# Optimization experiments

Measured on AMD Instinct MI355X. Metric: run time of the kernel, lower is better.

Reference implementation:

```python
import jax, jax.numpy as jnp
import numpy as np

HIDDEN = 4096
N_HEADS = 32
N_KV_HEADS = 8
HEAD_DIM = HIDDEN // N_HEADS  # 128
ROPE_THETA = 10000.0
B, S = 2, 2048


def apply_rope_neox(x, positions, theta=ROPE_THETA):
    # x: [B, S, H, D], positions: [S]
    d = x.shape[-1]
    inv_freq = 1.0 / (theta ** (jnp.arange(0, d, 2, dtype=jnp.float32) / d))  # [D/2]
    freqs = positions.astype(jnp.float32)[:, None] * inv_freq                # [S, D/2]
    cos = jnp.cos(freqs)[None, :, None, :]                                   # [1,S,1,D/2]
    sin = jnp.sin(freqs)[None, :, None, :]
    x1, x2 = x[..., : d // 2], x[..., d // 2 :]
    return jnp.concatenate([x1 * cos - x2 * sin, x2 * cos + x1 * sin], axis=-1).astype(x.dtype)


def setup_inputs() -> dict:
    key = jax.random.key(0)
    k1, k2, k3 = jax.random.split(key, 3)
    positions = jnp.arange(S, dtype=jnp.int64) if jax.config.jax_enable_x64 else jnp.arange(S, dtype=jnp.int32)
    hidden_states = jax.random.normal(k1, (B, S, HIDDEN), dtype=jnp.float32)
    q_size = N_HEADS * HEAD_DIM
    kv_size = N_KV_HEADS * HEAD_DIM
    w_qkv = jax.random.normal(k2, (HIDDEN, q_size + 2 * kv_size), dtype=jnp.float32) * (HIDDEN ** -0.5)
    w_o = jax.random.normal(k3, (q_size, HIDDEN), dtype=jnp.float32) * (q_size ** -0.5)
    return {"positions": positions, "hidden_states": hidden_states, "w_qkv": w_qkv, "w_o": w_o}


def reference(positions, hidden_states, w_qkv, w_o):
    q_size = N_HEADS * HEAD_DIM
    kv_size = N_KV_HEADS * HEAD_DIM
    scaling = HEAD_DIM ** -0.5

    # Fused QKV projection
    qkv = jnp.einsum('bsh,hm->bsm', hidden_states, w_qkv)
    q = qkv[..., :q_size].reshape(B, S, N_HEADS, HEAD_DIM)
    k = qkv[..., q_size : q_size + kv_size].reshape(B, S, N_KV_HEADS, HEAD_DIM)
    v = qkv[..., q_size + kv_size :].reshape(B, S, N_KV_HEADS, HEAD_DIM)

    # Neox-style RoPE on q, k
    q = apply_rope_neox(q, positions)
    k = apply_rope_neox(k, positions)

    # GQA: repeat kv heads to match query heads
    rep = N_HEADS // N_KV_HEADS
    k = jnp.repeat(k, rep, axis=2)  # [B,S,Hq,D]
    v = jnp.repeat(v, rep, axis=2)

    # Causal attention (prefill path of PagedAttention)
    scores = jnp.einsum('bqhd,bkhd->bhqk', q, k) * scaling  # [B,H,S,S]
    causal = jnp.tril(jnp.ones((S, S), dtype=bool))
    scores = jnp.where(causal[None, None], scores, jnp.finfo(scores.dtype).min)
    probs = jax.nn.softmax(scores, axis=-1)
    attn = jnp.einsum('bhqk,bkhd->bqhd', probs, v).reshape(B, S, q_size)

    # Output projection
    out = jnp.einsum('bsm,mh->bsh', attn, w_o)
    return out
```

## Files before the change

kernel.cpp:

```cpp
#include <hip/hip_runtime.h>

#define S_LEN 2048
#define NB 2
#define NH 32
#define NKV 8
#define HD 128
#define HID 4096
#define NQKV 6144

using bf16x8 = __attribute__((ext_vector_type(8))) __bf16;
using f32x4  = __attribute__((ext_vector_type(4))) float;

__device__ __forceinline__ ushort f2b(float f) {
  uint u = __builtin_bit_cast(uint, f);
  u += 0x7fffu + ((u >> 16) & 1u);
  return (ushort)(u >> 16);
}
__device__ __forceinline__ float b2f(ushort h) {
  uint u = ((uint)h) << 16;
  return __builtin_bit_cast(float, u);
}

__device__ __forceinline__ uint cvt_pk_bf16(float lo, float hi) {
  uint r;
  asm("v_cvt_pk_bf16_f32 %0, %1, %2" : "=v"(r) : "v"(lo), "v"(hi));
  return r;
}

__device__ __forceinline__ void gld16(const void* g, void* l) {
  __builtin_amdgcn_global_load_lds((const __attribute__((address_space(1))) void*)g,
                                   (__attribute__((address_space(3))) void*)l, 16, 0, 0);
}

__device__ __forceinline__ void stc(float* C, size_t i, float v)  { C[i] = v; }
__device__ __forceinline__ void stc(ushort* C, size_t i, float v) { C[i] = f2b(v); }

__global__ void cvt_bf16(const float* __restrict__ src, ushort* __restrict__ dst, int n) {
  int i = (blockIdx.x * 256 + threadIdx.x) * 4;
  if (i < n) {
    float4 v = *(const float4*)(src + i);
    *(ushort4*)(dst + i) = make_ushort4(f2b(v.x), f2b(v.y), f2b(v.z), f2b(v.w));
  }
}

__global__ void trans_f32_bf16(const float* __restrict__ src, ushort* __restrict__ dst,
                               int R, int C) {
  __shared__ float tile[32][33];
  const int c0 = blockIdx.x * 32, r0 = blockIdx.y * 32;
  const int x = threadIdx.x, y = threadIdx.y;
#pragma unroll
  for (int i = 0; i < 32; i += 8)
    tile[y + i][x] = src[(size_t)(r0 + y + i) * C + (c0 + x)];
  __syncthreads();
#pragma unroll
  for (int i = 0; i < 32; i += 8)
    dst[(size_t)(c0 + y + i) * R + (r0 + x)] = f2b(tile[x][y + i]);
}

template <typename OutT>
__global__ __launch_bounds__(256) void gemm_nt(const ushort* __restrict__ A,
                                               const ushort* __restrict__ Bt,
                                               OutT* __restrict__ C,
                                               int M, int N, int K, int lda, int ldb) {
  __shared__ ushort As[128 * 32];
  __shared__ ushort Bs[128 * 32];
  const int tid  = threadIdx.x;
  const int wave = tid >> 6;
  const int lane = tid & 63;
  const int lr = lane & 15, lg = lane >> 4;
  const int m0 = blockIdx.y * 128, n0 = blockIdx.x * 128;
  const int wm = (wave >> 1) * 64, wn = (wave & 1) * 64;

  f32x4 acc[4][4];
#pragma unroll
  for (int i = 0; i < 4; ++i)
#pragma unroll
    for (int j = 0; j < 4; ++j) acc[i][j] = (f32x4){0.f, 0.f, 0.f, 0.f};

  for (int kt = 0; kt < K; kt += 32) {
    __syncthreads();
#pragma unroll
    for (int it = 0; it < 2; ++it) {
      const int cbase = it * 256 + wave * 64;
      const int c = cbase + lane;
      const int row = c >> 2, kc = c & 3;
      gld16(A  + (size_t)(m0 + row) * lda + kt + kc * 8, As + cbase * 8);
      gld16(Bt + (size_t)(n0 + row) * ldb + kt + kc * 8, Bs + cbase * 8);
    }
    __syncthreads();
    bf16x8 af[4], bfg[4];
#pragma unroll
    for (int i = 0; i < 4; ++i) {
      af[i]  = *(const bf16x8*)(As + (wm + i * 16 + lr) * 32 + lg * 8);
      bfg[i] = *(const bf16x8*)(Bs + (wn + i * 16 + lr) * 32 + lg * 8);
    }
#pragma unroll
    for (int i = 0; i < 4; ++i)
#pragma unroll
      for (int j = 0; j < 4; ++j)
        acc[i][j] = __builtin_amdgcn_mfma_f32_16x16x32_bf16(af[i], bfg[j], acc[i][j], 0, 0, 0);
  }

#pragma unroll
  for (int i = 0; i < 4; ++i)
#pragma unroll
    for (int j = 0; j < 4; ++j)
#pragma unroll
      for (int r = 0; r < 4; ++r) {
        const int row = m0 + wm + i * 16 + lg * 4 + r;
        const int col = n0 + wn + j * 16 + lr;
        stc(C, (size_t)row * N + col, acc[i][j][r]);
      }
}

__global__ __launch_bounds__(256) void rope_qk(ushort* __restrict__ qkv) {
  int t = blockIdx.x * 256 + threadIdx.x;
  const int i = t & 63;
  t >>= 6;
  const int head  = t % (NH + NKV);
  const int token = t / (NH + NKV);
  const int s = token & (S_LEN - 1);
  const size_t base = (size_t)token * NQKV + (head < NH ? head * HD : HID + (head - NH) * HD);
  const float x1 = b2f(qkv[base + i]);
  const float x2 = b2f(qkv[base + 64 + i]);
  const float invf = exp2f(-(float)i * 0.2076205059304602f);
  const float fr = (float)s * invf;
  float cs, sn;
  sincosf(fr, &sn, &cs);
  float o1 = x1 * cs - x2 * sn;
  float o2 = x2 * cs + x1 * sn;
  if (head < NH) {
    o1 *= 0.08838834764831845f;
    o2 *= 0.08838834764831845f;
  }
  qkv[base + i]      = f2b(o1);
  qkv[base + 64 + i] = f2b(o2);
}

__global__ void vtrans(const ushort* __restrict__ qkv, ushort* __restrict__ Vt) {
  __shared__ ushort tile[32][33];
  const int dt = blockIdx.x * 32, st = blockIdx.y * 32, bk = blockIdx.z;
  const int b = bk >> 3, kv = bk & 7;
  const int x = threadIdx.x, y = threadIdx.y;
#pragma unroll
  for (int i = 0; i < 32; i += 8)
    tile[y + i][x] =
        qkv[(size_t)(b * S_LEN + st + y + i) * NQKV + 5120 + kv * HD + dt + x];
  __syncthreads();
#pragma unroll
  for (int i = 0; i < 32; i += 8)
    Vt[((size_t)bk * HD + dt + y + i) * S_LEN + st + x] = tile[x][y + i];
}

__global__ __launch_bounds__(256) void attn_fa(ushort* __restrict__ qkv,
                                               const ushort* __restrict__ Vt) {
  const int lin = blockIdx.x + 32 * blockIdx.y + 256 * blockIdx.z;
  const int swz = (lin & 7) * 64 + (lin >> 3);
  const int qp = swz & 31;
  const int g  = swz >> 5;
  const int kvh = g & 7;
  const int b   = g >> 3;

  const int wid  = threadIdx.x >> 6;
  const int lane = threadIdx.x & 63;
  const int lr = lane & 15, lg = lane >> 4;
  const int h  = kvh * 4 + wid;

  const ushort* K = qkv + (size_t)(b * S_LEN) * NQKV + HID + kvh * HD;
  const ushort* V = Vt + (size_t)(b * NKV + kvh) * (HD * S_LEN);

  __shared__ ushort P[4][2][16 * 40];

  for (int seg = 0; seg < 2; ++seg) {
    const int qt = seg ? (63 - qp) : qp;
    const int q0 = qt * 32;
    const ushort* Q = qkv + (size_t)(b * S_LEN + q0) * NQKV + h * HD;

    bf16x8 qf[2][4];
#pragma unroll
    for (int t = 0; t < 2; ++t)
#pragma unroll
      for (int kb = 0; kb < 4; ++kb)
        qf[t][kb] = *(const bf16x8*)(Q + (size_t)(t * 16 + lr) * NQKV + kb * 32 + lg * 8);

    f32x4 o[2][8];
#pragma unroll
    for (int t = 0; t < 2; ++t)
#pragma unroll
      for (int c = 0; c < 8; ++c) o[t][c] = (f32x4){0.f, 0.f, 0.f, 0.f};
    float mi[2]  = {-1e30f, -1e30f};
    float lip[2] = {0.f, 0.f};

    for (int k0 = 0; k0 <= q0; k0 += 32) {
      bf16x8 kf[2][4];
#pragma unroll
      for (int kb = 0; kb < 4; ++kb) {
        kf[0][kb] = *(const bf16x8*)(K + (size_t)(k0 + lr) * NQKV + kb * 32 + lg * 8);
        kf[1][kb] = *(const bf16x8*)(K + (size_t)(k0 + 16 + lr) * NQKV + kb * 32 + lg * 8);
      }
      bf16x8 vf[8];
#pragma unroll
      for (int c = 0; c < 8; ++c)
        vf[c] = *(const bf16x8*)(V + (size_t)(c * 16 + lr) * S_LEN + k0 + lg * 8);

      f32x4 s[2][2];
#pragma unroll
      for (int t = 0; t < 2; ++t)
#pragma unroll
        for (int u = 0; u < 2; ++u) s[t][u] = (f32x4){0.f, 0.f, 0.f, 0.f};

      __builtin_amdgcn_s_setprio(1);
#pragma unroll
      for (int kb = 0; kb < 4; ++kb) {
        s[0][0] = __builtin_amdgcn_mfma_f32_16x16x32_bf16(kf[0][kb], qf[0][kb], s[0][0], 0, 0, 0);
        s[1][0] = __builtin_amdgcn_mfma_f32_16x16x32_bf16(kf[0][kb], qf[1][kb], s[1][0], 0, 0, 0);
        s[0][1] = __builtin_amdgcn_mfma_f32_16x16x32_bf16(kf[1][kb], qf[0][kb], s[0][1], 0, 0, 0);
        s[1][1] = __builtin_amdgcn_mfma_f32_16x16x32_bf16(kf[1][kb], qf[1][kb], s[1][1], 0, 0, 0);
      }
      __builtin_amdgcn_s_setprio(0);

      if (k0 == q0) {
#pragma unroll
        for (int t = 0; t < 2; ++t)
#pragma unroll
          for (int u = 0; u < 2; ++u)
#pragma unroll
            for (int r = 0; r < 4; ++r)
              if (u * 16 + lg * 4 + r > t * 16 + lr) s[t][u][r] = -1e30f;
      }

      float pm[2];
#pragma unroll
      for (int t = 0; t < 2; ++t) {
        float a = fmaxf(fmaxf(s[t][0][0], s[t][0][1]), fmaxf(s[t][0][2], s[t][0][3]));
        float c = fmaxf(fmaxf(s[t][1][0], s[t][1][1]), fmaxf(s[t][1][2], s[t][1][3]));
        pm[t] = fmaxf(a, c);
      }

      if (__any((pm[0] > mi[0] + 8.f) || (pm[1] > mi[1] + 8.f))) {
#pragma unroll
        for (int t = 0; t < 2; ++t) {
          float m = pm[t];
          m = fmaxf(m, __shfl_xor(m, 16));
          m = fmaxf(m, __shfl_xor(m, 32));
          const float mn = fmaxf(mi[t], m);
          const float al = __expf(mi[t] - mn);
          mi[t] = mn;
          lip[t] *= al;
#pragma unroll
          for (int r = 0; r < 4; ++r) {
            const float ar = __shfl(al, lg * 4 + r);
#pragma unroll
            for (int c = 0; c < 8; ++c) o[t][c][r] *= ar;
          }
        }
      }

#pragma unroll
      for (int t = 0; t < 2; ++t) {
        float p[2][4];
#pragma unroll
        for (int u = 0; u < 2; ++u)
#pragma unroll
          for (int r = 0; r < 4; ++r) p[u][r] = __expf(s[t][u][r] - mi[t]);
        lip[t] += ((p[0][0] + p[0][1]) + (p[0][2] + p[0][3])) +
                  ((p[1][0] + p[1][1]) + (p[1][2] + p[1][3]));
        ushort* Pw = &P[wid][t][0];
#pragma unroll
        for (int u = 0; u < 2; ++u) {
          const uint w0 = cvt_pk_bf16(p[u][0], p[u][1]);
          const uint w1 = cvt_pk_bf16(p[u][2], p[u][3]);
          *(uint2*)(Pw + lr * 40 + u * 16 + lg * 4) = make_uint2(w0, w1);
        }
      }
      const bf16x8 pa0 = *(const bf16x8*)(&P[wid][0][0] + lr * 40 + lg * 8);
      const bf16x8 pa1 = *(const bf16x8*)(&P[wid][1][0] + lr * 40 + lg * 8);

      __builtin_amdgcn_s_setprio(1);
#pragma unroll
      for (int c = 0; c < 8; ++c) {
        o[0][c] = __builtin_amdgcn_mfma_f32_16x16x32_bf16(pa0, vf[c], o[0][c], 0, 0, 0);
        o[1][c] = __builtin_amdgcn_mfma_f32_16x16x32_bf16(pa1, vf[c], o[1][c], 0, 0, 0);
      }
      __builtin_amdgcn_s_setprio(0);
    }

    float linv[2];
#pragma unroll
    for (int t = 0; t < 2; ++t) {
      float rt = lip[t];
      rt += __shfl_xor(rt, 16);
      rt += __shfl_xor(rt, 32);
      linv[t] = 1.f / rt;
    }
#pragma unroll
    for (int t = 0; t < 2; ++t) {
#pragma unroll
      for (int r = 0; r < 4; ++r) {
        const float ir = __shfl(linv[t], lg * 4 + r);
        const size_t row = (size_t)(b * S_LEN + q0 + t * 16 + lg * 4 + r) * NQKV + h * HD;
#pragma unroll
        for (int c = 0; c < 8; ++c) qkv[row + c * 16 + lr] = f2b(o[t][c][r] * ir);
      }
    }
  }
}

extern "C" void kernel_launch(void* const* d_in, const int* in_sizes, int n_in,
                              void* d_out, int out_size, void* d_ws, size_t ws_size,
                              hipStream_t stream) {
  const float* hidden = (const float*)d_in[1];
  const float* w_qkv  = (const float*)d_in[2];
  const float* w_o    = (const float*)d_in[3];
  float* out = (float*)d_out;
  char* ws = (char*)d_ws;

  ushort* wqkvT = (ushort*)(ws);
  ushort* Vt    = (ushort*)(ws);
  ushort* hb    = (ushort*)(ws + (48u << 20));
  ushort* woT   = (ushort*)(ws + (48u << 20));
  ushort* qkvb  = (ushort*)(ws + (80u << 20));

  trans_f32_bf16<<<dim3(192, 128), dim3(32, 8), 0, stream>>>(w_qkv, wqkvT, HID, NQKV);
  cvt_bf16<<<16384, 256, 0, stream>>>(hidden, hb, NB * S_LEN * HID);
  gemm_nt<ushort><<<dim3(48, 32), 256, 0, stream>>>(
      hb, wqkvT, qkvb, NB * S_LEN, NQKV, HID, HID, HID);
  rope_qk<<<40960, 256, 0, stream>>>(qkvb);
  vtrans<<<dim3(4, 64, 16), dim3(32, 8), 0, stream>>>(qkvb, Vt);
  trans_f32_bf16<<<dim3(128, 128), dim3(32, 8), 0, stream>>>(w_o, woT, HID, HID);
  attn_fa<<<dim3(32, 8, 2), 256, 0, stream>>>(qkvb, Vt);
  gemm_nt<float><<<dim3(32, 32), 256, 0, stream>>>(
      qkvb, woT, out, NB * S_LEN, HID, HID, NQKV, HID);
}
```

Before: 953.3 us.

## Rewrite GEMM with double-buffered LDS, 128x256 tiles, swizzle, and XCD remap

Replaces the single-buffered 128x128 GEMM with a 512-thread 128x256-tile kernel. It double-buffers the LDS panels so the next K slice loads while MFMAs run, XOR-swizzles the LDS chunk layout to cut bank conflicts, and remaps workgroup IDs so neighbouring tiles land on the same XCD for L2 reuse. It also raises wave priority around the MFMA bursts. The costs are more LDS per block and a possibly lower tile count, fewer CUs busy, on the smaller output projection.

New measurement: 959.5 us. About the same (+0.6%).

```diff
diff --git a/kernel.cpp b/kernel.cpp
--- a/kernel.cpp
+++ b/kernel.cpp
@@ -57,19 +57,35 @@
     dst[(size_t)(c0 + y + i) * R + (r0 + x)] = f2b(tile[x][y + i]);
 }
 
+__device__ __forceinline__ void stage_panel(const ushort* __restrict__ src, int ld,
+                                            int row0, int kt, ushort* dst,
+                                            int nchunks, int wave, int lane) {
+  for (int cb = wave * 64; cb < nchunks; cb += 512) {
+    const int c = cb + lane;
+    const int row = c >> 2;
+    const int cg = (c & 3) ^ (row & 3);
+    gld16(src + (size_t)(row0 + row) * ld + kt + cg * 8, dst + cb * 8);
+  }
+}
+
 template <typename OutT>
-__global__ __launch_bounds__(256) void gemm_nt(const ushort* __restrict__ A,
-                                               const ushort* __restrict__ Bt,
-                                               OutT* __restrict__ C,
-                                               int M, int N, int K, int lda, int ldb) {
-  __shared__ ushort As[128 * 32];
-  __shared__ ushort Bs[128 * 32];
-  const int tid  = threadIdx.x;
-  const int wave = tid >> 6;
-  const int lane = tid & 63;
+__global__ __launch_bounds__(512, 4) void gemm_np(const ushort* __restrict__ A,
+                                                  const ushort* __restrict__ Bt,
+                                                  OutT* __restrict__ C,
+                                                  int M, int Ncol, int K,
+                                                  int lda, int ldb) {
+  __shared__ ushort As[2][128 * 32];
+  __shared__ ushort Bs[2][256 * 32];
+  const int tid = threadIdx.x, wave = tid >> 6, lane = tid & 63;
   const int lr = lane & 15, lg = lane >> 4;
-  const int m0 = blockIdx.y * 128, n0 = blockIdx.x * 128;
-  const int wm = (wave >> 1) * 64, wn = (wave & 1) * 64;
+  const int wm = wave >> 2, wn = wave & 3;
+
+  const int gx = gridDim.x;
+  const int nwg = gx * gridDim.y;
+  const int orig = blockIdx.y * gx + blockIdx.x;
+  const int q8 = nwg >> 3, r8 = nwg & 7, xcd = orig & 7, loc = orig >> 3;
+  const int wg = (xcd < r8 ? xcd * (q8 + 1) : r8 * (q8 + 1) + (xcd - r8) * q8) + loc;
+  const int n0 = (wg % gx) * 256, m0 = (wg / gx) * 128;
 
   f32x4 acc[4][4];
 #pragma unroll
@@ -77,28 +93,46 @@
 #pragma unroll
     for (int j = 0; j < 4; ++j) acc[i][j] = (f32x4){0.f, 0.f, 0.f, 0.f};
 
-  for (int kt = 0; kt < K; kt += 32) {
-    __syncthreads();
-#pragma unroll
-    for (int it = 0; it < 2; ++it) {
-      const int cbase = it * 256 + wave * 64;
-      const int c = cbase + lane;
-      const int row = c >> 2, kc = c & 3;
-      gld16(A  + (size_t)(m0 + row) * lda + kt + kc * 8, As + cbase * 8);
-      gld16(Bt + (size_t)(n0 + row) * ldb + kt + kc * 8, Bs + cbase * 8);
-    }
-    __syncthreads();
-    bf16x8 af[4], bfg[4];
-#pragma unroll
-    for (int i = 0; i < 4; ++i) {
-      af[i]  = *(const bf16x8*)(As + (wm + i * 16 + lr) * 32 + lg * 8);
-      bfg[i] = *(const bf16x8*)(Bs + (wn + i * 16 + lr) * 32 + lg * 8);
-    }
-#pragma unroll
-    for (int i = 0; i < 4; ++i)
-#pragma unroll
-      for (int j = 0; j < 4; ++j)
-        acc[i][j] = __builtin_amdgcn_mfma_f32_16x16x32_bf16(af[i], bfg[j], acc[i][j], 0, 0, 0);
+  const int foff = lr * 32 + ((lg ^ (lr & 3)) << 3);
+  const int NT = K >> 5;
+
+  stage_panel(A,  lda, m0, 0, As[0], 512, wave, lane);
+  stage_panel(Bt, ldb, n0, 0, Bs[0], 1024, wave, lane);
+  asm volatile("s_waitcnt vmcnt(0)" ::: "memory");
+  __builtin_amdgcn_s_barrier();
+
+  for (int it = 0; it < NT; ++it) {
+    const int buf = it & 1;
+    const bool more = (it + 1 < NT);
+    if (more) {
+      stage_panel(A,  lda, m0, (it + 1) << 5, As[buf ^ 1], 512, wave, lane);
+      stage_panel(Bt, ldb, n0, (it + 1) << 5, Bs[buf ^ 1], 1024, wave, lane);
+    }
+    const ushort* Ap = As[buf] + wm * (64 * 32);
+    const ushort* Bp = Bs[buf] + wn * (64 * 32);
+#pragma unroll
+    for (int q = 0; q < 4; ++q) {
+      const int qm = q & 1, qn = q >> 1;
+      bf16x8 af[2], bfr[2];
+#pragma unroll
+      for (int f = 0; f < 2; ++f)
+        af[f] = *(const bf16x8*)(Ap + (qm * 2 + f) * (16 * 32) + foff);
+#pragma unroll
+      for (int g = 0; g < 2; ++g)
+        bfr[g] = *(const bf16x8*)(Bp + (qn * 2 + g) * (16 * 32) + foff);
+      __builtin_amdgcn_s_setprio(1);
+#pragma unroll
+      for (int f = 0; f < 2; ++f)
+#pragma unroll
+        for (int g = 0; g < 2; ++g)
+          acc[qm * 2 + f][qn * 2 + g] = __builtin_amdgcn_mfma_f32_16x16x32_bf16(
+              af[f], bfr[g], acc[qm * 2 + f][qn * 2 + g], 0, 0, 0);
+      __builtin_amdgcn_s_setprio(0);
+    }
+    if (more) {
+      asm volatile("s_waitcnt vmcnt(0)" ::: "memory");
+      __builtin_amdgcn_s_barrier();
+    }
   }
 
 #pragma unroll
@@ -107,9 +141,9 @@
     for (int j = 0; j < 4; ++j)
 #pragma unroll
       for (int r = 0; r < 4; ++r) {
-        const int row = m0 + wm + i * 16 + lg * 4 + r;
-        const int col = n0 + wn + j * 16 + lr;
-        stc(C, (size_t)row * N + col, acc[i][j][r]);
+        const int row = m0 + wm * 64 + i * 16 + lg * 4 + r;
+        const int col = n0 + wn * 64 + j * 16 + lr;
+        stc(C, (size_t)row * Ncol + col, acc[i][j][r]);
       }
 }
 
@@ -323,12 +357,12 @@
 
   trans_f32_bf16<<<dim3(192, 128), dim3(32, 8), 0, stream>>>(w_qkv, wqkvT, HID, NQKV);
   cvt_bf16<<<16384, 256, 0, stream>>>(hidden, hb, NB * S_LEN * HID);
-  gemm_nt<ushort><<<dim3(48, 32), 256, 0, stream>>>(
+  gemm_np<ushort><<<dim3(24, 32), 512, 0, stream>>>(
       hb, wqkvT, qkvb, NB * S_LEN, NQKV, HID, HID, HID);
   rope_qk<<<40960, 256, 0, stream>>>(qkvb);
   vtrans<<<dim3(4, 64, 16), dim3(32, 8), 0, stream>>>(qkvb, Vt);
   trans_f32_bf16<<<dim3(128, 128), dim3(32, 8), 0, stream>>>(w_o, woT, HID, HID);
   attn_fa<<<dim3(32, 8, 2), 256, 0, stream>>>(qkvb, Vt);
-  gemm_nt<float><<<dim3(32, 32), 256, 0, stream>>>(
+  gemm_np<float><<<dim3(16, 32), 512, 0, stream>>>(
       qkvb, woT, out, NB * S_LEN, HID, HID, NQKV, HID);
 }
```

## Double-buffer GEMM LDS tiles with K=64 stages and XOR-swizzled layout

Applied to the files above, without the earlier changes.

Replaces the single-buffered K=32 GEMM with a double-buffered K=64 version. Global-to-LDS loads for the next tile are issued before compute on the current one, with a partial vmcnt wait and raw barriers in place of two __syncthreads per step. The LDS layout is XOR-swizzled to avoid bank conflicts, and MFMA issue gets a raised wave priority. LDS use grows to 64KB per block, which may limit occupancy, and the hand-placed waitcnt is fragile.

Result: faster. 855.4 us (-10.3%).

```diff
diff --git a/kernel.cpp b/kernel.cpp
--- a/kernel.cpp
+++ b/kernel.cpp
@@ -57,19 +57,33 @@
     dst[(size_t)(c0 + y + i) * R + (r0 + x)] = f2b(tile[x][y + i]);
 }
 
+__device__ __forceinline__ void stage_tile(const ushort* __restrict__ A,
+                                           const ushort* __restrict__ Bt,
+                                           int lda, int ldb, int m0, int n0, int kt,
+                                           ushort* dA, ushort* dB, int wave, int lane) {
+#pragma unroll
+  for (int h = 0; h < 4; ++h) {
+    const int cb = h * 256 + wave * 64;
+    const int c = cb + lane;
+    const int row = c >> 3;
+    const int kc = (c & 7) ^ (row & 7);
+    gld16(A  + (size_t)(m0 + row) * lda + kt + kc * 8, dA + cb * 8);
+    gld16(Bt + (size_t)(n0 + row) * ldb + kt + kc * 8, dB + cb * 8);
+  }
+}
+
 template <typename OutT>
-__global__ __launch_bounds__(256) void gemm_nt(const ushort* __restrict__ A,
-                                               const ushort* __restrict__ Bt,
-                                               OutT* __restrict__ C,
-                                               int M, int N, int K, int lda, int ldb) {
-  __shared__ ushort As[128 * 32];
-  __shared__ ushort Bs[128 * 32];
-  const int tid  = threadIdx.x;
-  const int wave = tid >> 6;
-  const int lane = tid & 63;
+__global__ __launch_bounds__(256, 2) void gemm_p2(const ushort* __restrict__ A,
+                                                  const ushort* __restrict__ Bt,
+                                                  OutT* __restrict__ C,
+                                                  int M, int Ncol, int K,
+                                                  int lda, int ldb) {
+  __shared__ ushort As[2][128 * 64];
+  __shared__ ushort Bs[2][128 * 64];
+  const int tid = threadIdx.x, wave = tid >> 6, lane = tid & 63;
   const int lr = lane & 15, lg = lane >> 4;
+  const int wm = wave >> 1, wn = wave & 1;
   const int m0 = blockIdx.y * 128, n0 = blockIdx.x * 128;
-  const int wm = (wave >> 1) * 64, wn = (wave & 1) * 64;
 
   f32x4 acc[4][4];
 #pragma unroll
@@ -77,39 +91,54 @@
 #pragma unroll
     for (int j = 0; j < 4; ++j) acc[i][j] = (f32x4){0.f, 0.f, 0.f, 0.f};
 
-  for (int kt = 0; kt < K; kt += 32) {
-    __syncthreads();
-#pragma unroll
-    for (int it = 0; it < 2; ++it) {
-      const int cbase = it * 256 + wave * 64;
-      const int c = cbase + lane;
-      const int row = c >> 2, kc = c & 3;
-      gld16(A  + (size_t)(m0 + row) * lda + kt + kc * 8, As + cbase * 8);
-      gld16(Bt + (size_t)(n0 + row) * ldb + kt + kc * 8, Bs + cbase * 8);
-    }
-    __syncthreads();
-    bf16x8 af[4], bfg[4];
-#pragma unroll
-    for (int i = 0; i < 4; ++i) {
-      af[i]  = *(const bf16x8*)(As + (wm + i * 16 + lr) * 32 + lg * 8);
-      bfg[i] = *(const bf16x8*)(Bs + (wn + i * 16 + lr) * 32 + lg * 8);
-    }
-#pragma unroll
-    for (int i = 0; i < 4; ++i)
-#pragma unroll
-      for (int j = 0; j < 4; ++j)
-        acc[i][j] = __builtin_amdgcn_mfma_f32_16x16x32_bf16(af[i], bfg[j], acc[i][j], 0, 0, 0);
-  }
-
-#pragma unroll
-  for (int i = 0; i < 4; ++i)
-#pragma unroll
-    for (int j = 0; j < 4; ++j)
+  const int NT = K >> 6;
+
+  stage_tile(A, Bt, lda, ldb, m0, n0, 0, As[0], Bs[0], wave, lane);
+
+  for (int it = 0; it < NT; ++it) {
+    const int buf = it & 1;
+    if (it + 1 < NT) {
+      stage_tile(A, Bt, lda, ldb, m0, n0, (it + 1) << 6, As[buf ^ 1], Bs[buf ^ 1],
+                 wave, lane);
+      asm volatile("s_waitcnt vmcnt(8)" ::: "memory");
+    } else {
+      asm volatile("s_waitcnt vmcnt(0)" ::: "memory");
+    }
+    asm volatile("s_barrier" ::: "memory");
+
+#pragma unroll
+    for (int kk = 0; kk < 2; ++kk) {
+      bf16x8 af[4], bfr[4];
+#pragma unroll
+      for (int f = 0; f < 4; ++f) {
+        const int row = wm * 64 + f * 16 + lr;
+        af[f] = *(const bf16x8*)(&As[buf][row * 64 + (((kk * 4 + lg) ^ (lr & 7)) << 3)]);
+      }
+#pragma unroll
+      for (int g = 0; g < 4; ++g) {
+        const int row = wn * 64 + g * 16 + lr;
+        bfr[g] = *(const bf16x8*)(&Bs[buf][row * 64 + (((kk * 4 + lg) ^ (lr & 7)) << 3)]);
+      }
+      __builtin_amdgcn_s_setprio(1);
+#pragma unroll
+      for (int f = 0; f < 4; ++f)
+#pragma unroll
+        for (int g = 0; g < 4; ++g)
+          acc[f][g] = __builtin_amdgcn_mfma_f32_16x16x32_bf16(af[f], bfr[g], acc[f][g], 0, 0, 0);
+      __builtin_amdgcn_s_setprio(0);
+    }
+    asm volatile("s_barrier" ::: "memory");
+  }
+
+#pragma unroll
+  for (int f = 0; f < 4; ++f)
+#pragma unroll
+    for (int g = 0; g < 4; ++g)
 #pragma unroll
       for (int r = 0; r < 4; ++r) {
-        const int row = m0 + wm + i * 16 + lg * 4 + r;
-        const int col = n0 + wn + j * 16 + lr;
-        stc(C, (size_t)row * N + col, acc[i][j][r]);
+        const int row = m0 + wm * 64 + f * 16 + lg * 4 + r;
+        const int col = n0 + wn * 64 + g * 16 + lr;
+        stc(C, (size_t)row * Ncol + col, acc[f][g][r]);
       }
 }
 
@@ -323,12 +352,12 @@
 
   trans_f32_bf16<<<dim3(192, 128), dim3(32, 8), 0, stream>>>(w_qkv, wqkvT, HID, NQKV);
   cvt_bf16<<<16384, 256, 0, stream>>>(hidden, hb, NB * S_LEN * HID);
-  gemm_nt<ushort><<<dim3(48, 32), 256, 0, stream>>>(
+  gemm_p2<ushort><<<dim3(48, 32), 256, 0, stream>>>(
       hb, wqkvT, qkvb, NB * S_LEN, NQKV, HID, HID, HID);
   rope_qk<<<40960, 256, 0, stream>>>(qkvb);
   vtrans<<<dim3(4, 64, 16), dim3(32, 8), 0, stream>>>(qkvb, Vt);
   trans_f32_bf16<<<dim3(128, 128), dim3(32, 8), 0, stream>>>(w_o, woT, HID, HID);
   attn_fa<<<dim3(32, 8, 2), 256, 0, stream>>>(qkvb, Vt);
-  gemm_nt<float><<<dim3(32, 32), 256, 0, stream>>>(
+  gemm_p2<float><<<dim3(32, 32), 256, 0, stream>>>(
       qkvb, woT, out, NB * S_LEN, HID, HID, NQKV, HID);
 }
```
